# Optimization experiments

Measured on AMD Instinct MI355X. Metric: run time of the kernel, lower is better.

Reference implementation:

```python
import jax, jax.numpy as jnp
import numpy as np

EMB = 768
HEADS = 8

def setup_inputs() -> dict:
    key = jax.random.key(0)
    ks = jax.random.split(key, 5)
    x = jax.random.normal(ks[0], (8, 2048, EMB), dtype=jnp.float32)
    s = 1.0 / np.sqrt(EMB)
    W_qkv = jax.random.normal(ks[1], (EMB, 3 * EMB), dtype=jnp.float32) * s
    b_qkv = jnp.zeros((3 * EMB,), dtype=jnp.float32)
    W_proj = jax.random.normal(ks[2], (EMB, EMB), dtype=jnp.float32) * s
    b_proj = jnp.zeros((EMB,), dtype=jnp.float32)
    return {"x": x, "W_qkv": W_qkv, "b_qkv": b_qkv, "W_proj": W_proj, "b_proj": b_proj}

def reference(x, W_qkv, b_qkv, W_proj, b_proj):
    B, N, E = x.shape
    H = HEADS
    D = E // H
    qkv = x @ W_qkv + b_qkv  # [B, N, 3E]
    q, k, v = jnp.split(qkv, 3, axis=-1)
    # [B, N, E] -> [B, H, N, D]
    def heads(t):
        return t.reshape(B, N, H, D).transpose(0, 2, 1, 3)
    q, k, v = heads(q), heads(k), heads(v)
    # NOTE: original scales by 1/sqrt(emb_size), not 1/sqrt(head_dim)
    dots = jnp.einsum('bhnd,bhmd->bhnm', q, k) / jnp.sqrt(jnp.float32(E))
    attn = jax.nn.softmax(dots, axis=-1)  # dropout inactive (eval mode)
    out = jnp.einsum('bhnm,bhmd->bhnd', attn, v)
    out = out.transpose(0, 2, 1, 3).reshape(B, N, E)
    return out @ W_proj + b_proj
```

## Files before the change

kernel.cpp:

```cpp
#include <hip/hip_runtime.h>
#include <hip/hip_bf16.h>

typedef __attribute__((ext_vector_type(8))) short bf16x8;
typedef __attribute__((ext_vector_type(4))) short bf16x4;
typedef __attribute__((ext_vector_type(4))) float f32x4;
typedef __attribute__((ext_vector_type(16))) float f32x16;
typedef __attribute__((ext_vector_type(4))) unsigned int uint4v;

__device__ __forceinline__ short f2bf(float f) {
    unsigned int u = __float_as_uint(f);
    u += 0x7FFFu + ((u >> 16) & 1u);
    return (short)(u >> 16);
}

__device__ __forceinline__ unsigned cvtpk(float lo, float hi) {
    unsigned r;
    asm("v_cvt_pk_bf16_f32 %0, %1, %2" : "=v"(r) : "v"(lo), "v"(hi));
    return r;
}

__device__ __forceinline__ void gload_lds16(const void* g, void* l) {
    __builtin_amdgcn_global_load_lds(
        (const __attribute__((address_space(1))) void*)g,
        (__attribute__((address_space(3))) void*)l, 16, 0, 0);
}

__global__ __launch_bounds__(256) void cast_kernel(const float* __restrict__ in,
                                                   short* __restrict__ out, int n4) {
    int i = blockIdx.x * 256 + threadIdx.x;
    if (i >= n4) return;
    const f32x4 v = *(const f32x4*)(in + (size_t)i * 4);
    bf16x4 o;
    o[0] = f2bf(v[0]); o[1] = f2bf(v[1]); o[2] = f2bf(v[2]); o[3] = f2bf(v[3]);
    *(bf16x4*)(out + (size_t)i * 4) = o;
}

__global__ __launch_bounds__(256) void transpose_cast_kernel(const float* __restrict__ W,
                                                             short* __restrict__ WT,
                                                             int R, int C) {
    __shared__ float tile[64][65];
    const int bc = blockIdx.x * 64;
    const int br = blockIdx.y * 64;
    const int t = threadIdx.x;
#pragma unroll
    for (int i = 0; i < 16; ++i) {
        int o = t + 256 * i;
        int r = o >> 6, c = o & 63;
        tile[r][c] = W[(size_t)(br + r) * C + bc + c];
    }
    __syncthreads();
#pragma unroll
    for (int i = 0; i < 16; ++i) {
        int o = t + 256 * i;
        int c = o >> 6, r = o & 63;
        WT[(size_t)(bc + c) * R + br + r] = f2bf(tile[r][c]);
    }
}

__global__ __launch_bounds__(256, 3) void gemm1_kernel(
    const short* __restrict__ A, const short* __restrict__ BT,
    const float* __restrict__ bias,
    short* __restrict__ Qh, short* __restrict__ Kh, short* __restrict__ Vt)
{
    __shared__ short As[128][64];
    __shared__ short Bs[128][64];
    const int K = 768;
    const int t = threadIdx.x;
    const int w = t >> 6, l = t & 63;
    const int wr = w >> 1, wc = w & 1;
    const int lr = l & 15, lg = l >> 4;

    const int srow = w * 32 + (l >> 3);
    const int scol = (l & 7) * 8;
    const short* Ag = A + (size_t)blockIdx.x * 128 * K + (size_t)srow * K + scol;
    const short* Bg = BT + (size_t)blockIdx.y * 128 * K + (size_t)srow * K + scol;

    const f32x4 z4 = {0.f, 0.f, 0.f, 0.f};
    f32x4 acc[4][4];
#pragma unroll
    for (int i = 0; i < 4; ++i)
#pragma unroll
        for (int j = 0; j < 4; ++j) acc[i][j] = z4;

    for (int kt = 0; kt < K; kt += 64) {
#pragma unroll
        for (int i = 0; i < 4; ++i) {
            gload_lds16(Ag + kt + (size_t)(i * 8) * K, &As[w * 32 + i * 8][0]);
            gload_lds16(Bg + kt + (size_t)(i * 8) * K, &Bs[w * 32 + i * 8][0]);
        }
        __syncthreads();
#pragma unroll
        for (int kk = 0; kk < 2; ++kk) {
            bf16x8 af[4], bfr[4];
#pragma unroll
            for (int mi = 0; mi < 4; ++mi)
                af[mi] = *(const bf16x8*)&As[wr * 64 + mi * 16 + lr][kk * 32 + lg * 8];
#pragma unroll
            for (int ni = 0; ni < 4; ++ni)
                bfr[ni] = *(const bf16x8*)&Bs[wc * 64 + ni * 16 + lr][kk * 32 + lg * 8];
#pragma unroll
            for (int mi = 0; mi < 4; ++mi)
#pragma unroll
                for (int ni = 0; ni < 4; ++ni)
                    acc[mi][ni] = __builtin_amdgcn_mfma_f32_16x16x32_bf16(
                        af[mi], bfr[ni], acc[mi][ni], 0, 0, 0);
        }
        __syncthreads();
    }

    const float qs = 0.05205877f;
    const int rb = blockIdx.x * 128 + wr * 64;
    const int cb = blockIdx.y * 128 + wc * 64;
#pragma unroll
    for (int ni = 0; ni < 4; ++ni) {
        const int c = cb + ni * 16 + lr;
        const float bv = bias[c];
        const int which = (c >= 1536) ? 2 : (c >= 768 ? 1 : 0);
        const int cc = c - which * 768;
        const int h = cc / 96;
        const int d = cc - h * 96;
#pragma unroll
        for (int mi = 0; mi < 4; ++mi) {
            const int r0 = rb + mi * 16 + lg * 4;
            const int b = r0 >> 11, n0 = r0 & 2047;
            const int hb = b * 8 + h;
            if (which == 2) {
                bf16x4 pk;
#pragma unroll
                for (int r = 0; r < 4; ++r) pk[r] = f2bf(acc[mi][ni][r] + bv);
                const int ktile = n0 >> 6;
                const int s = (((n0 & 63) >> 3) ^ (d & 7));
                *(bf16x4*)&Vt[((size_t)(hb * 32 + ktile) * 96 + d) * 64 + s * 8 + (n0 & 7)] = pk;
            } else if (which == 1) {
#pragma unroll
                for (int r = 0; r < 4; ++r)
                    Kh[((size_t)hb * 2048 + n0 + r) * 104 + d] = f2bf(acc[mi][ni][r] + bv);
            } else {
#pragma unroll
                for (int r = 0; r < 4; ++r)
                    Qh[((size_t)hb * 2048 + n0 + r) * 96 + d] = f2bf((acc[mi][ni][r] + bv) * qs);
            }
        }
    }
}

__global__ __launch_bounds__(256, 3) void attn_kernel(
    const short* __restrict__ Qh, const short* __restrict__ Kh,
    const short* __restrict__ Vt, short* __restrict__ AO)
{
    __shared__ __align__(16) char smem[51200];
    short (*K0)[104] = (short (*)[104])smem;
    short (*K1)[104] = (short (*)[104])(smem + 13312);
    short* V0 = (short*)(smem + 26624);
    short* V1 = (short*)(smem + 38912);
    short (*Qs)[96] = (short (*)[96])smem;
    float (*ltab)[32] = (float (*)[32])smem;

    const int t = threadIdx.x;
    const int w = t >> 6, l = t & 63;
    const int ql = l & 31, hi = l >> 5;

    const unsigned L = blockIdx.y * 16 + blockIdx.x;
    const int bh = (int)((L & 7) + 8 * (L >> 7));
    const int qt = (int)((L >> 3) & 15);

    const short* Qg  = Qh + ((size_t)bh * 2048 + (size_t)qt * 128) * 96;
    const short* Kgp = Kh + (size_t)bh * 2048 * 104;
    const short* Vgt = Vt + (size_t)bh * 32 * 6144;

#pragma unroll
    for (int j = 0; j < 6; ++j) {
        const int idx = j * 4 + w;
        gload_lds16(Qg + idx * 512 + l * 8, smem + idx * 1024);
    }
    __syncthreads();
    bf16x8 qf[6];
#pragma unroll
    for (int kk = 0; kk < 6; ++kk)
        qf[kk] = *(const bf16x8*)&Qs[w * 32 + ql][kk * 16 + hi * 8];
    __syncthreads();

    auto stageK = [&](int kt, short (*wK)[104]) {
        const short* s = Kgp + kt * 6656 + l * 8;
#pragma unroll
        for (int j = 0; j < 4; ++j) {
            const int idx = j * 4 + w;
            if (idx < 13) gload_lds16(s + idx * 512, (char*)wK + idx * 1024);
        }
    };
    auto stageV = [&](int kt, short* wV) {
        const short* s = Vgt + kt * 6144 + l * 8;
#pragma unroll
        for (int j = 0; j < 3; ++j) {
            const int idx = j * 4 + w;
            gload_lds16(s + idx * 512, (char*)wV + idx * 1024);
        }
    };

    stageK(0, K0);
    stageV(0, V0);
    __syncthreads();

    f32x16 oacc[3];
#pragma unroll
    for (int i = 0; i < 3; ++i)
#pragma unroll
        for (int r = 0; r < 16; ++r) oacc[i][r] = 0.f;
    float lacc = 0.f;

    auto iter = [&](int kt, short (*rK)[104], const short* rV,
                    short (*wK)[104], short* wV) {
        if (kt < 31) { stageK(kt + 1, wK); stageV(kt + 1, wV); }

#pragma unroll
        for (int h = 0; h < 2; ++h) {
            f32x16 sa;
#pragma unroll
            for (int r = 0; r < 16; ++r) sa[r] = 0.f;
            __builtin_amdgcn_s_setprio(1);
#pragma unroll
            for (int kk = 0; kk < 6; ++kk) {
                bf16x8 kf = *(const bf16x8*)&rK[h * 32 + ql][kk * 16 + hi * 8];
                sa = __builtin_amdgcn_mfma_f32_32x32x16_bf16(kf, qf[kk], sa, 0, 0, 0);
            }
            __builtin_amdgcn_s_setprio(0);

            float p[16];
#pragma unroll
            for (int r = 0; r < 16; ++r) {
                p[r] = __builtin_amdgcn_exp2f(sa[r]);
                lacc += p[r];
            }
            unsigned x0 = cvtpk(p[0], p[1]),   y0 = cvtpk(p[4], p[5]);
            unsigned x1 = cvtpk(p[2], p[3]),   y1 = cvtpk(p[6], p[7]);
            unsigned x2 = cvtpk(p[8], p[9]),   y2 = cvtpk(p[12], p[13]);
            unsigned x3 = cvtpk(p[10], p[11]), y3 = cvtpk(p[14], p[15]);
            asm("v_permlane32_swap_b32 %0, %1" : "+v"(x0), "+v"(y0));
            asm("v_permlane32_swap_b32 %0, %1" : "+v"(x1), "+v"(y1));
            asm("v_permlane32_swap_b32 %0, %1" : "+v"(x2), "+v"(y2));
            asm("v_permlane32_swap_b32 %0, %1" : "+v"(x3), "+v"(y3));
            uint4v uA; uA[0] = x0; uA[1] = x1; uA[2] = y0; uA[3] = y1;
            uint4v uB; uB[0] = x2; uB[1] = x3; uB[2] = y2; uB[3] = y3;
            bf16x8 pa0 = __builtin_bit_cast(bf16x8, uA);
            bf16x8 pa1 = __builtin_bit_cast(bf16x8, uB);

            __builtin_amdgcn_s_setprio(1);
#pragma unroll
            for (int kb = 0; kb < 2; ++kb) {
                const int c = (h * 2 + kb) * 2 + hi;
                const bf16x8 paf = kb ? pa1 : pa0;
#pragma unroll
                for (int db = 0; db < 3; ++db) {
                    const int row = db * 32 + ql;
                    bf16x8 vf = *(const bf16x8*)&rV[row * 64 + ((c ^ (row & 7)) << 3)];
                    oacc[db] = __builtin_amdgcn_mfma_f32_32x32x16_bf16(paf, vf, oacc[db], 0, 0, 0);
                }
            }
            __builtin_amdgcn_s_setprio(0);
        }
        __syncthreads();
    };

    for (int kt = 0; kt < 32; kt += 2) {
        iter(kt,     K0, V0, K1, V1);
        iter(kt + 1, K1, V1, K0, V0);
    }

    float lsum = lacc + __shfl_xor(lacc, 32);
    if (l < 32) ltab[w][l] = lsum;
    asm volatile("s_waitcnt lgkmcnt(0)" ::: "memory");

    float linv[16];
#pragma unroll
    for (int r = 0; r < 16; ++r) {
        const int q = (r & 3) + 8 * (r >> 2) + 4 * hi;
        linv[r] = 1.0f / ltab[w][q];
    }

    const int b = bh >> 3, h2 = bh & 7;
    const size_t rowbase = (size_t)b * 2048 + qt * 128 + w * 32;
#pragma unroll
    for (int db = 0; db < 3; ++db) {
#pragma unroll
        for (int r = 0; r < 16; ++r) {
            const int q = (r & 3) + 8 * (r >> 2) + 4 * hi;
            AO[(rowbase + q) * 768 + h2 * 96 + db * 32 + ql] = f2bf(oacc[db][r] * linv[r]);
        }
    }
}

__global__ __launch_bounds__(256, 3) void gemm2_kernel(
    const short* __restrict__ A, const short* __restrict__ BT,
    const float* __restrict__ bias, float* __restrict__ out)
{
    __shared__ short As[128][64];
    __shared__ short Bs[128][64];
    const int K = 768;
    const int t = threadIdx.x;
    const int w = t >> 6, l = t & 63;
    const int wr = w >> 1, wc = w & 1;
    const int lr = l & 15, lg = l >> 4;

    const int srow = w * 32 + (l >> 3);
    const int scol = (l & 7) * 8;
    const short* Ag = A + (size_t)blockIdx.x * 128 * K + (size_t)srow * K + scol;
    const short* Bg = BT + (size_t)blockIdx.y * 128 * K + (size_t)srow * K + scol;

    const f32x4 z4 = {0.f, 0.f, 0.f, 0.f};
    f32x4 acc[4][4];
#pragma unroll
    for (int i = 0; i < 4; ++i)
#pragma unroll
        for (int j = 0; j < 4; ++j) acc[i][j] = z4;

    for (int kt = 0; kt < K; kt += 64) {
#pragma unroll
        for (int i = 0; i < 4; ++i) {
            gload_lds16(Ag + kt + (size_t)(i * 8) * K, &As[w * 32 + i * 8][0]);
            gload_lds16(Bg + kt + (size_t)(i * 8) * K, &Bs[w * 32 + i * 8][0]);
        }
        __syncthreads();
#pragma unroll
        for (int kk = 0; kk < 2; ++kk) {
            bf16x8 af[4], bfr[4];
#pragma unroll
            for (int mi = 0; mi < 4; ++mi)
                af[mi] = *(const bf16x8*)&As[wr * 64 + mi * 16 + lr][kk * 32 + lg * 8];
#pragma unroll
            for (int ni = 0; ni < 4; ++ni)
                bfr[ni] = *(const bf16x8*)&Bs[wc * 64 + ni * 16 + lr][kk * 32 + lg * 8];
#pragma unroll
            for (int mi = 0; mi < 4; ++mi)
#pragma unroll
                for (int ni = 0; ni < 4; ++ni)
                    acc[mi][ni] = __builtin_amdgcn_mfma_f32_16x16x32_bf16(
                        af[mi], bfr[ni], acc[mi][ni], 0, 0, 0);
        }
        __syncthreads();
    }

    const int rb = blockIdx.x * 128 + wr * 64;
    const int cb = blockIdx.y * 128 + wc * 64;
#pragma unroll
    for (int ni = 0; ni < 4; ++ni) {
        const int c = cb + ni * 16 + lr;
        const float bv = bias[c];
#pragma unroll
        for (int mi = 0; mi < 4; ++mi) {
            const int r0 = rb + mi * 16 + lg * 4;
#pragma unroll
            for (int r = 0; r < 4; ++r)
                out[(size_t)(r0 + r) * 768 + c] = acc[mi][ni][r] + bv;
        }
    }
}

extern "C" void kernel_launch(void* const* d_in, const int* in_sizes, int n_in,
                              void* d_out, int out_size, void* d_ws, size_t ws_size,
                              hipStream_t stream) {
    const float* x     = (const float*)d_in[0];
    const float* Wqkv  = (const float*)d_in[1];
    const float* bqkv  = (const float*)d_in[2];
    const float* Wproj = (const float*)d_in[3];
    const float* bproj = (const float*)d_in[4];
    float* out = (float*)d_out;

    char* ws = (char*)d_ws;
    short* xb     = (short*)(ws);
    short* WqkvT  = (short*)(ws + 25165824);
    short* WprojT = (short*)(ws + 28704768);
    short* Qh     = (short*)(ws + 29884416);
    short* Kh     = (short*)(ws + 55050240);
    short* Vt     = (short*)(ws + 82313216);
    short* AO     = xb;

    cast_kernel<<<12288, 256, 0, stream>>>(x, xb, 3145728);
    transpose_cast_kernel<<<dim3(36, 12), 256, 0, stream>>>(Wqkv, WqkvT, 768, 2304);
    transpose_cast_kernel<<<dim3(12, 12), 256, 0, stream>>>(Wproj, WprojT, 768, 768);
    gemm1_kernel<<<dim3(128, 18), 256, 0, stream>>>(xb, WqkvT, bqkv, Qh, Kh, Vt);
    attn_kernel<<<dim3(16, 64), 256, 0, stream>>>(Qh, Kh, Vt, AO);
    gemm2_kernel<<<dim3(128, 6), 256, 0, stream>>>(AO, WprojT, bproj, out);
}
```

Before: 239.5 us.

## Double-buffer LDS tiles in both projection GEMMs to overlap loads with MFMA

Both GEMM kernels now use two LDS buffers per operand and issue the async global-to-LDS loads for the next K tile before computing on the current one, so memory latency overlaps with MFMA work. LDS use per block doubles to 64KB and the occupancy hint drops from 3 to 2 blocks per CU. Fewer resident blocks may cut latency hiding from wave-level parallelism. The GEMMs are only part of the total time, next to the attention kernel.

```diff
diff --git a/kernel.cpp b/kernel.cpp
--- a/kernel.cpp
+++ b/kernel.cpp
@@ -57,13 +57,13 @@
     }
 }
 
-__global__ __launch_bounds__(256, 3) void gemm1_kernel(
+__global__ __launch_bounds__(256, 2) void gemm1_kernel(
     const short* __restrict__ A, const short* __restrict__ BT,
     const float* __restrict__ bias,
     short* __restrict__ Qh, short* __restrict__ Kh, short* __restrict__ Vt)
 {
-    __shared__ short As[128][64];
-    __shared__ short Bs[128][64];
+    __shared__ short As[2][128][64];
+    __shared__ short Bs[2][128][64];
     const int K = 768;
     const int t = threadIdx.x;
     const int w = t >> 6, l = t & 63;
@@ -82,22 +82,23 @@
 #pragma unroll
         for (int j = 0; j < 4; ++j) acc[i][j] = z4;
 
-    for (int kt = 0; kt < K; kt += 64) {
+    auto stage = [&](int kt, int buf) {
 #pragma unroll
         for (int i = 0; i < 4; ++i) {
-            gload_lds16(Ag + kt + (size_t)(i * 8) * K, &As[w * 32 + i * 8][0]);
-            gload_lds16(Bg + kt + (size_t)(i * 8) * K, &Bs[w * 32 + i * 8][0]);
-        }
-        __syncthreads();
+            gload_lds16(Ag + kt * 64 + (size_t)(i * 8) * K, &As[buf][w * 32 + i * 8][0]);
+            gload_lds16(Bg + kt * 64 + (size_t)(i * 8) * K, &Bs[buf][w * 32 + i * 8][0]);
+        }
+    };
+    auto compute = [&](int buf) {
 #pragma unroll
         for (int kk = 0; kk < 2; ++kk) {
             bf16x8 af[4], bfr[4];
 #pragma unroll
             for (int mi = 0; mi < 4; ++mi)
-                af[mi] = *(const bf16x8*)&As[wr * 64 + mi * 16 + lr][kk * 32 + lg * 8];
+                af[mi] = *(const bf16x8*)&As[buf][wr * 64 + mi * 16 + lr][kk * 32 + lg * 8];
 #pragma unroll
             for (int ni = 0; ni < 4; ++ni)
-                bfr[ni] = *(const bf16x8*)&Bs[wc * 64 + ni * 16 + lr][kk * 32 + lg * 8];
+                bfr[ni] = *(const bf16x8*)&Bs[buf][wc * 64 + ni * 16 + lr][kk * 32 + lg * 8];
 #pragma unroll
             for (int mi = 0; mi < 4; ++mi)
 #pragma unroll
@@ -105,6 +106,16 @@
                     acc[mi][ni] = __builtin_amdgcn_mfma_f32_16x16x32_bf16(
                         af[mi], bfr[ni], acc[mi][ni], 0, 0, 0);
         }
+    };
+
+    stage(0, 0);
+    __syncthreads();
+    for (int kt = 0; kt < 12; kt += 2) {
+        stage(kt + 1, 1);
+        compute(0);
+        __syncthreads();
+        if (kt + 2 < 12) stage(kt + 2, 0);
+        compute(1);
         __syncthreads();
     }
 
@@ -289,12 +300,12 @@
     }
 }
 
-__global__ __launch_bounds__(256, 3) void gemm2_kernel(
+__global__ __launch_bounds__(256, 2) void gemm2_kernel(
     const short* __restrict__ A, const short* __restrict__ BT,
     const float* __restrict__ bias, float* __restrict__ out)
 {
-    __shared__ short As[128][64];
-    __shared__ short Bs[128][64];
+    __shared__ short As[2][128][64];
+    __shared__ short Bs[2][128][64];
     const int K = 768;
     const int t = threadIdx.x;
     const int w = t >> 6, l = t & 63;
@@ -313,22 +324,23 @@
 #pragma unroll
         for (int j = 0; j < 4; ++j) acc[i][j] = z4;
 
-    for (int kt = 0; kt < K; kt += 64) {
+    auto stage = [&](int kt, int buf) {
 #pragma unroll
         for (int i = 0; i < 4; ++i) {
-            gload_lds16(Ag + kt + (size_t)(i * 8) * K, &As[w * 32 + i * 8][0]);
-            gload_lds16(Bg + kt + (size_t)(i * 8) * K, &Bs[w * 32 + i * 8][0]);
-        }
-        __syncthreads();
+            gload_lds16(Ag + kt * 64 + (size_t)(i * 8) * K, &As[buf][w * 32 + i * 8][0]);
+            gload_lds16(Bg + kt * 64 + (size_t)(i * 8) * K, &Bs[buf][w * 32 + i * 8][0]);
+        }
+    };
+    auto compute = [&](int buf) {
 #pragma unroll
         for (int kk = 0; kk < 2; ++kk) {
             bf16x8 af[4], bfr[4];
 #pragma unroll
             for (int mi = 0; mi < 4; ++mi)
-                af[mi] = *(const bf16x8*)&As[wr * 64 + mi * 16 + lr][kk * 32 + lg * 8];
+                af[mi] = *(const bf16x8*)&As[buf][wr * 64 + mi * 16 + lr][kk * 32 + lg * 8];
 #pragma unroll
             for (int ni = 0; ni < 4; ++ni)
-                bfr[ni] = *(const bf16x8*)&Bs[wc * 64 + ni * 16 + lr][kk * 32 + lg * 8];
+                bfr[ni] = *(const bf16x8*)&Bs[buf][wc * 64 + ni * 16 + lr][kk * 32 + lg * 8];
 #pragma unroll
             for (int mi = 0; mi < 4; ++mi)
 #pragma unroll
@@ -336,6 +348,16 @@
                     acc[mi][ni] = __builtin_amdgcn_mfma_f32_16x16x32_bf16(
                         af[mi], bfr[ni], acc[mi][ni], 0, 0, 0);
         }
+    };
+
+    stage(0, 0);
+    __syncthreads();
+    for (int kt = 0; kt < 12; kt += 2) {
+        stage(kt + 1, 1);
+        compute(0);
+        __syncthreads();
+        if (kt + 2 < 12) stage(kt + 2, 0);
+        compute(1);
         __syncthreads();
     }
 
```

New measurement: 279.2 us. 1.17x slower.
